# Kernel tuning notes

Hardware: AMD Instinct MI355X
Metric: run time of the kernel (lower is better)

Reference implementation:

```python
import jax, jax.numpy as jnp
import numpy as np

B, L, D, K = 16, 512, 512, 8
D2 = 2 * D
KS = 9
PAD = (KS - 1) // 2
EPS = 1e-5


def _conv_block(x, w, b, g, beta):
    # x: [B, L, D]; conv over time dim with 'same' padding, then LayerNorm over D, ReLU
    y = jax.lax.conv_general_dilated(
        x.transpose(0, 2, 1), w, window_strides=(1,), padding=[(PAD, PAD)],
        dimension_numbers=('NCH', 'OIH', 'NCH'))
    y = y.transpose(0, 2, 1) + b  # [B, L, D]
    mean = jnp.mean(y, axis=-1, keepdims=True)
    var = jnp.var(y, axis=-1, keepdims=True)
    y = (y - mean) * jax.lax.rsqrt(var + EPS) * g + beta
    return jax.nn.relu(y)


def _gru_scan(x, w_ih, w_hh, b_ih, b_hh):
    # x: [B, L, D]; torch GRUCell math, input = concat(x_t, h_{t-1}) per module
    def step(h, x_t):
        p = jnp.concatenate([x_t, h], axis=-1)          # [B, D + D2]
        gi = p @ w_ih.T + b_ih                          # [B, 3*D2]
        gh = h @ w_hh.T + b_hh
        ir, iz, inn = jnp.split(gi, 3, axis=-1)
        hr, hz, hn = jnp.split(gh, 3, axis=-1)
        r = jax.nn.sigmoid(ir + hr)
        z = jax.nn.sigmoid(iz + hz)
        n = jnp.tanh(inn + r * hn)
        h_new = (1.0 - z) * n + z * h
        return h_new, h_new

    h0 = jnp.zeros((x.shape[0], w_hh.shape[1]), x.dtype)
    _, hs = jax.lax.scan(step, h0, x.transpose(1, 0, 2))  # [L, B, D2]
    return hs.transpose(1, 0, 2)                           # [B, L, D2]


def setup_inputs() -> dict:
    key = jax.random.key(0)
    ks = jax.random.split(key, 12)
    n = lambda k, sh, s=0.02: jax.random.normal(k, sh, dtype=jnp.float32) * s
    return {
        'h_text': jax.random.normal(ks[0], (B, L, D), dtype=jnp.float32),
        'conv1_w': n(ks[1], (D, D, KS)), 'conv1_b': jnp.zeros((D,), jnp.float32),
        'ln1_g': jnp.ones((D,), jnp.float32), 'ln1_b': jnp.zeros((D,), jnp.float32),
        'conv2_w': n(ks[2], (D, D, KS)), 'conv2_b': jnp.zeros((D,), jnp.float32),
        'ln2_g': jnp.ones((D,), jnp.float32), 'ln2_b': jnp.zeros((D,), jnp.float32),
        'w_ih': n(ks[3], (3 * D2, D + D2)), 'w_hh': n(ks[4], (3 * D2, D2)),
        'b_ih': jnp.zeros((3 * D2,), jnp.float32), 'b_hh': jnp.zeros((3 * D2,), jnp.float32),
        'mdn_w_w': n(ks[5], (K, D2)), 'mdn_w_b': jnp.zeros((K,), jnp.float32),
        'mdn_sigma_w': n(ks[6], (K * D2, D2)), 'mdn_sigma_b': jnp.zeros((K * D2,), jnp.float32),
        'mdn_mu_w': n(ks[7], (K * D2, D2)), 'mdn_mu_b': jnp.zeros((K * D2,), jnp.float32),
    }


def reference(h_text, conv1_w, conv1_b, ln1_g, ln1_b, conv2_w, conv2_b, ln2_g, ln2_b,
              w_ih, w_hh, b_ih, b_hh, mdn_w_w, mdn_w_b, mdn_sigma_w, mdn_sigma_b,
              mdn_mu_w, mdn_mu_b):
    x = _conv_block(h_text, conv1_w, conv1_b, ln1_g, ln1_b)
    x = _conv_block(x, conv2_w, conv2_b, ln2_g, ln2_b)
    h = _gru_scan(x, w_ih, w_hh, b_ih, b_hh)                 # [B, L, 2D]
    w = jax.nn.softmax(h @ mdn_w_w.T + mdn_w_b, axis=-1)     # [B, L, K]
    sigma = jnp.exp(h @ mdn_sigma_w.T + mdn_sigma_b).reshape(B, L, K, D2)
    mu = (h @ mdn_mu_w.T + mdn_mu_b).reshape(B, L, K, D2)
    return (w, sigma, mu)
```

## Files before the change

### kernel.cpp

```cpp
#include <hip/hip_runtime.h>
#include <hip/hip_bf16.h>
#include <math.h>

#define BB 16
#define LL 512
#define DD 512
#define DD2 1024
#define KMIX 8
#define LPAD 520
#define GRU_KSTEPS 33

typedef __attribute__((ext_vector_type(8))) short short8;
typedef __attribute__((ext_vector_type(4))) float f32x4;
typedef unsigned short ushort;

__device__ __forceinline__ float bf2f(ushort u) {
  union { float f; unsigned i; } v; v.i = ((unsigned)u) << 16; return v.f;
}
__device__ __forceinline__ ushort f2bf(float f) {
  union { float f; unsigned i; } v; v.f = f;
  unsigned i = v.i;
  unsigned r = i + 0x7FFF + ((i >> 16) & 1);
  return (ushort)(r >> 16);
}

__global__ void k_zero_bf16(ushort* p, long n) {
  for (long i = blockIdx.x * 256 + threadIdx.x; i < n; i += (long)gridDim.x * 256) p[i] = 0;
}
__global__ void k_fill_xpad(const float* __restrict__ x, ushort* __restrict__ xp) {
  const long n = (long)BB * LPAD * DD;
  for (long i = blockIdx.x * 256 + threadIdx.x; i < n; i += (long)gridDim.x * 256) {
    int d = (int)(i & 511);
    long rest = i >> 9;
    int p = (int)(rest % LPAD);
    int b = (int)(rest / LPAD);
    float v = 0.f;
    if (p >= 4 && p < 516) v = x[((long)b * LL + (p - 4)) * DD + d];
    xp[i] = f2bf(v);
  }
}
__global__ void k_pack_convw(const float* __restrict__ w, ushort* __restrict__ wp) {
  const long n = (long)DD * DD * 9;
  for (long idx = blockIdx.x * 256 + threadIdx.x; idx < n; idx += (long)gridDim.x * 256) {
    int i = (int)(idx & 511);
    int o = (int)((idx >> 9) & 511);
    int k = (int)(idx >> 18);
    wp[idx] = f2bf(w[((long)o * DD + i) * 9 + k]);
  }
}
__global__ void k_pack_wihx(const float* __restrict__ w_ih, ushort* __restrict__ wp) {
  const long n = (long)3 * DD2 * DD;
  for (long idx = blockIdx.x * 256 + threadIdx.x; idx < n; idx += (long)gridDim.x * 256) {
    int i = (int)(idx & 511);
    int nr = (int)(idx >> 9);
    wp[idx] = f2bf(w_ih[(long)nr * 1536 + i]);
  }
}
__global__ void k_pack_bf16(const float* __restrict__ s, ushort* __restrict__ d, long n) {
  for (long i = blockIdx.x * 256 + threadIdx.x; i < n; i += (long)gridDim.x * 256) d[i] = f2bf(s[i]);
}
__global__ void k_pack_gru(const float* __restrict__ w_ih, const float* __restrict__ w_hh,
                           const float* __restrict__ b_hh, ushort* __restrict__ wp) {
  const long n = (long)64 * 6 * GRU_KSTEPS * 64 * 8;
  for (long idx = blockIdx.x * 256 + threadIdx.x; idx < n; idx += (long)gridDim.x * 256) {
    int j = (int)(idx & 7);
    int lane = (int)((idx >> 3) & 63);
    long r9 = idx >> 9;
    int ks = (int)(r9 % GRU_KSTEPS);
    long tmp = r9 / GRU_KSTEPS;
    int s = (int)(tmp % 6);
    int blk = (int)(tmp / 6);
    int k = ks * 32 + ((lane >> 4) << 3) + j;
    int u = blk * 16 + (lane & 15);
    float v = 0.f;
    if (s < 3) {
      if (k < 1024) v = w_ih[((long)(s * DD2 + u)) * 1536 + 512 + k];
    } else {
      int nr = (s - 3) * DD2 + u;
      if (k < 1024) v = w_hh[(long)nr * DD2 + k];
      else if (k == 1024) v = b_hh[nr];
    }
    wp[idx] = f2bf(v);
  }
}
__global__ void k_init_hbuf(ushort* hb, unsigned* flags) {
  int i = blockIdx.x * 256 + threadIdx.x;
  if (i < 16384) hb[i] = 0;
  if (i < 1024) flags[i] = 0u;
}

template <int MODE, int AMAP>
__global__ __launch_bounds__(256) void gemm128(
    const ushort* __restrict__ A, int lda, long segAoff,
    const ushort* __restrict__ Bt, int ldb, long segBoff,
    int nseg, int kseg, void* __restrict__ Cout, int ldc,
    const float* __restrict__ bias) {
  __shared__ ushort As[128 * 64];
  __shared__ ushort Bs[128 * 64];
  const int tid = threadIdx.x, lane = tid & 63, w = tid >> 6;
  const int wr = w >> 1, wc = w & 1;
  const int m0 = blockIdx.y * 128, n0 = blockIdx.x * 128;

  const ushort* Abase;
  if (AMAP == 1) {
    int b = m0 >> 9, l = m0 & 511;
    Abase = A + ((long)(b * LPAD + l)) * DD;
  } else {
    Abase = A + (long)m0 * lda;
  }
  const ushort* Bbase = Bt + (long)n0 * ldb;

  f32x4 acc[4][4];
#pragma unroll
  for (int i = 0; i < 4; i++)
#pragma unroll
    for (int j = 0; j < 4; j++) acc[i][j] = {0.f, 0.f, 0.f, 0.f};

  for (int seg = 0; seg < nseg; ++seg) {
    const ushort* Aseg = Abase + (long)seg * segAoff;
    const ushort* Bseg = Bbase + (long)seg * segBoff;
    for (int k0 = 0; k0 < kseg; k0 += 64) {
#pragma unroll
      for (int it = 0; it < 4; ++it) {
        int chunk = it * 256 + tid;
        int r = chunk >> 3, cc = chunk & 7;
        int sc = cc ^ (r & 7);
        *(short8*)&As[(size_t)chunk * 8] = *(const short8*)(Aseg + (long)r * lda + k0 + sc * 8);
        *(short8*)&Bs[(size_t)chunk * 8] = *(const short8*)(Bseg + (long)r * ldb + k0 + sc * 8);
      }
      __syncthreads();
#pragma unroll
      for (int kk = 0; kk < 2; ++kk) {
        short8 af[4], bfv[4];
#pragma unroll
        for (int m = 0; m < 4; m++) {
          int row = wr * 64 + m * 16 + (lane & 15);
          int ch = (kk * 4 + (lane >> 4)) ^ (row & 7);
          af[m] = *(const short8*)&As[(size_t)(row * 8 + ch) * 8];
        }
#pragma unroll
        for (int nn = 0; nn < 4; nn++) {
          int row = wc * 64 + nn * 16 + (lane & 15);
          int ch = (kk * 4 + (lane >> 4)) ^ (row & 7);
          bfv[nn] = *(const short8*)&Bs[(size_t)(row * 8 + ch) * 8];
        }
#pragma unroll
        for (int m = 0; m < 4; m++)
#pragma unroll
          for (int nn = 0; nn < 4; nn++)
            acc[m][nn] = __builtin_amdgcn_mfma_f32_16x16x32_bf16(af[m], bfv[nn], acc[m][nn], 0, 0, 0);
      }
      __syncthreads();
    }
  }
  float bvals[4];
#pragma unroll
  for (int nn = 0; nn < 4; nn++) {
    int c = n0 + wc * 64 + nn * 16 + (lane & 15);
    bvals[nn] = bias[c];
  }
#pragma unroll
  for (int m = 0; m < 4; m++) {
    int rbase = m0 + wr * 64 + m * 16 + ((lane >> 4) << 2);
#pragma unroll
    for (int nn = 0; nn < 4; nn++) {
      int c = n0 + wc * 64 + nn * 16 + (lane & 15);
#pragma unroll
      for (int j = 0; j < 4; j++) {
        float v = acc[m][nn][j] + bvals[nn];
        long off = (long)(rbase + j) * ldc + c;
        if (MODE == 0) ((float*)Cout)[off] = v;
        else if (MODE == 1) ((ushort*)Cout)[off] = f2bf(v);
        else if (MODE == 2) ((float*)Cout)[off] = v;
        else ((float*)Cout)[off] = expf(v);
      }
    }
  }
}

template <int DSTPAD>
__global__ __launch_bounds__(256) void ln_relu(
    const float* __restrict__ y, const float* __restrict__ g,
    const float* __restrict__ be, ushort* __restrict__ dst) {
  const int r = blockIdx.x, tid = threadIdx.x;
  float v0 = y[(long)r * DD + tid];
  float v1 = y[(long)r * DD + 256 + tid];
  float s = v0 + v1, sq = v0 * v0 + v1 * v1;
#pragma unroll
  for (int o = 32; o; o >>= 1) { s += __shfl_down(s, o); sq += __shfl_down(sq, o); }
  __shared__ float red[8];
  int w = tid >> 6, lane = tid & 63;
  if (lane == 0) { red[w] = s; red[4 + w] = sq; }
  __syncthreads();
  if (tid == 0) {
    float ts = 0.f, tq = 0.f;
#pragma unroll
    for (int i = 0; i < 4; i++) { ts += red[i]; tq += red[4 + i]; }
    red[0] = ts; red[1] = tq;
  }
  __syncthreads();
  float mean = red[0] * (1.f / 512.f);
  float var = red[1] * (1.f / 512.f) - mean * mean;
  float rs = rsqrtf(var + 1e-5f);
  long dbase;
  if (DSTPAD) { int b = r >> 9, l = r & 511; dbase = ((long)(b * LPAD + l + 4)) * DD; }
  else dbase = (long)r * DD;
  float o0 = fmaxf(0.f, (v0 - mean) * rs * g[tid] + be[tid]);
  float o1 = fmaxf(0.f, (v1 - mean) * rs * g[tid + 256] + be[tid + 256]);
  dst[dbase + tid] = f2bf(o0);
  dst[dbase + 256 + tid] = f2bf(o1);
}

__global__ __launch_bounds__(256, 1) void gru_scan(
    const ushort* __restrict__ Wp, const ushort* __restrict__ gix,
    const float* __restrict__ b_hh,
    ushort* __restrict__ hbuf, ushort* __restrict__ h_seq,
    unsigned* __restrict__ flags) {
  __shared__ float red[4 * 6 * 256];
  const int tid = threadIdx.x, lane = tid & 63, w = tid >> 6, blk = blockIdx.x;
  const int j_c = w;
  const int u_local = lane & 15;
  const int b = ((lane >> 4) << 2) + j_c;
  const int u = (blk << 4) + u_local;
  const int lanep = ((blk & 1) * 2 + (u_local >> 3)) * 16 + b;
  const long hout_off = ((long)(blk >> 1) * 64 + lanep) * 8 + (u_local & 7);
  const ushort* wpw = Wp + (long)blk * 6 * GRU_KSTEPS * 512 + (long)lane * 8;
  const float bhr = b_hh[u], bhz = b_hh[DD2 + u], bhn = b_hh[2 * DD2 + u];
  float hold = 0.f;

  short8 wreg0[8], wreg1[8], wreg2[8];
#pragma unroll
  for (int i = 0; i < 8; ++i) {
    const int ks = i * 4 + w;
    wreg0[i] = *(const short8*)(wpw + (long)(0 * GRU_KSTEPS + ks) * 512);
    wreg1[i] = *(const short8*)(wpw + (long)(1 * GRU_KSTEPS + ks) * 512);
    wreg2[i] = *(const short8*)(wpw + (long)(2 * GRU_KSTEPS + ks) * 512);
  }

  for (int t = 0; t < LL; ++t) {
    const long gr = ((long)b * LL + t) * 3072 + u;
    const float gx_r = bf2f(__builtin_nontemporal_load(gix + gr));
    const float gx_z = bf2f(__builtin_nontemporal_load(gix + gr + DD2));
    const float gx_n = bf2f(__builtin_nontemporal_load(gix + gr + 2 * DD2));

    if (t > 0) {
      if (w == 0) {
        const unsigned tgt = (unsigned)t;
        while (1) {
          unsigned f = __hip_atomic_load(&flags[lane << 4], __ATOMIC_RELAXED,
                                         __HIP_MEMORY_SCOPE_AGENT);
          if (__all((int)(f >= tgt))) break;
          __builtin_amdgcn_s_sleep(1);
        }
      }
      __syncthreads();
    }

    const ushort* hb = hbuf + ((long)t << 14);
    f32x4 acc0 = {0.f,0.f,0.f,0.f}, acc1 = acc0, acc2 = acc0,
          acc3 = acc0, acc4 = acc0, acc5 = acc0;
#pragma unroll
    for (int i = 0; i < 8; ++i) {
      const int ks = i * 4 + w;
      unsigned long long* ap = (unsigned long long*)(hb + (((long)ks * 64 + lane) << 3));
      union { unsigned long long q[2]; short8 v; } cv;
      cv.q[0] = __hip_atomic_load(ap,     __ATOMIC_RELAXED, __HIP_MEMORY_SCOPE_AGENT);
      cv.q[1] = __hip_atomic_load(ap + 1, __ATOMIC_RELAXED, __HIP_MEMORY_SCOPE_AGENT);
      short8 b3 = *(const short8*)(wpw + (long)(3 * GRU_KSTEPS + ks) * 512);
      short8 b4 = *(const short8*)(wpw + (long)(4 * GRU_KSTEPS + ks) * 512);
      short8 b5 = *(const short8*)(wpw + (long)(5 * GRU_KSTEPS + ks) * 512);
      acc0 = __builtin_amdgcn_mfma_f32_16x16x32_bf16(cv.v, wreg0[i], acc0, 0, 0, 0);
      acc1 = __builtin_amdgcn_mfma_f32_16x16x32_bf16(cv.v, wreg1[i], acc1, 0, 0, 0);
      acc2 = __builtin_amdgcn_mfma_f32_16x16x32_bf16(cv.v, wreg2[i], acc2, 0, 0, 0);
      acc3 = __builtin_amdgcn_mfma_f32_16x16x32_bf16(cv.v, b3, acc3, 0, 0, 0);
      acc4 = __builtin_amdgcn_mfma_f32_16x16x32_bf16(cv.v, b4, acc4, 0, 0, 0);
      acc5 = __builtin_amdgcn_mfma_f32_16x16x32_bf16(cv.v, b5, acc5, 0, 0, 0);
    }
#pragma unroll
    for (int j = 0; j < 4; ++j) {
      red[((w * 6 + 0) << 8) + (j << 6) + lane] = acc0[j];
      red[((w * 6 + 1) << 8) + (j << 6) + lane] = acc1[j];
      red[((w * 6 + 2) << 8) + (j << 6) + lane] = acc2[j];
      red[((w * 6 + 3) << 8) + (j << 6) + lane] = acc3[j];
      red[((w * 6 + 4) << 8) + (j << 6) + lane] = acc4[j];
      red[((w * 6 + 5) << 8) + (j << 6) + lane] = acc5[j];
    }
    __syncthreads();
    float v0 = 0.f, v1 = 0.f, v2 = 0.f, v3 = 0.f, v4 = 0.f, v5 = 0.f;
#pragma unroll
    for (int wv = 0; wv < 4; ++wv) {
      const int base = ((wv * 6) << 8) + (j_c << 6) + lane;
      v0 += red[base];
      v1 += red[base + 256];
      v2 += red[base + 512];
      v3 += red[base + 768];
      v4 += red[base + 1024];
      v5 += red[base + 1280];
    }
    const float rg = 1.f / (1.f + __expf(-(gx_r + v0 + v3 + bhr)));
    const float zg = 1.f / (1.f + __expf(-(gx_z + v1 + v4 + bhz)));
    const float nx = gx_n + v2 + rg * (v5 + bhn);
    const float ng = 1.f - 2.f / (__expf(2.f * nx) + 1.f);
    const float hn = (1.f - zg) * ng + zg * hold;
    hold = hn;
    const ushort h16 = f2bf(hn);
    h_seq[((long)b * LL + t) * DD2 + u] = h16;
    if (t < LL - 1) {
      __hip_atomic_store(hbuf + (((long)(t + 1)) << 14) + hout_off, h16,
                         __ATOMIC_RELAXED, __HIP_MEMORY_SCOPE_AGENT);
      __syncthreads();
      if (tid == 0)
        __hip_atomic_store(&flags[blk << 4], (unsigned)(t + 1), __ATOMIC_RELAXED,
                           __HIP_MEMORY_SCOPE_AGENT);
    }
  }
}

__global__ __launch_bounds__(256) void w_head(
    const ushort* __restrict__ h_seq, const float* __restrict__ ww,
    const float* __restrict__ wb, float* __restrict__ out) {
  const int tid = threadIdx.x, lane = tid & 63, w = tid >> 6;
  const long r = (long)blockIdx.x * 4 + w;
  float s[KMIX];
#pragma unroll
  for (int k = 0; k < KMIX; k++) s[k] = 0.f;
  for (int u = lane; u < DD2; u += 64) {
    float hv = bf2f(h_seq[r * DD2 + u]);
#pragma unroll
    for (int k = 0; k < KMIX; k++) s[k] += hv * ww[(long)k * DD2 + u];
  }
#pragma unroll
  for (int k = 0; k < KMIX; k++)
#pragma unroll
    for (int o = 32; o; o >>= 1) s[k] += __shfl_xor(s[k], o);
#pragma unroll
  for (int k = 0; k < KMIX; k++) s[k] += wb[k];
  float m = s[0];
#pragma unroll
  for (int k = 1; k < KMIX; k++) m = fmaxf(m, s[k]);
  float esum = 0.f;
#pragma unroll
  for (int k = 0; k < KMIX; k++) { s[k] = expf(s[k] - m); esum += s[k]; }
  float mine = 0.f;
#pragma unroll
  for (int k = 0; k < KMIX; k++) if (lane == k) mine = s[k];
  if (lane < KMIX) out[r * KMIX + lane] = mine / esum;
}

extern "C" void kernel_launch(void* const* d_in, const int* in_sizes, int n_in,
                              void* d_out, int out_size, void* d_ws, size_t ws_size,
                              hipStream_t stream) {
  const float* h_text     = (const float*)d_in[0];
  const float* conv1_w    = (const float*)d_in[1];
  const float* conv1_b    = (const float*)d_in[2];
  const float* ln1_g      = (const float*)d_in[3];
  const float* ln1_b      = (const float*)d_in[4];
  const float* conv2_w    = (const float*)d_in[5];
  const float* conv2_b    = (const float*)d_in[6];
  const float* ln2_g      = (const float*)d_in[7];
  const float* ln2_b      = (const float*)d_in[8];
  const float* w_ih       = (const float*)d_in[9];
  const float* w_hh       = (const float*)d_in[10];
  const float* b_ih       = (const float*)d_in[11];
  const float* b_hh       = (const float*)d_in[12];
  const float* mdn_w_w    = (const float*)d_in[13];
  const float* mdn_w_b    = (const float*)d_in[14];
  const float* mdn_sig_w  = (const float*)d_in[15];
  const float* mdn_sig_b  = (const float*)d_in[16];
  const float* mdn_mu_w   = (const float*)d_in[17];
  const float* mdn_mu_b   = (const float*)d_in[18];
  float* out = (float*)d_out;

  char* ws = (char*)d_ws;
  size_t off = 0;
  auto take = [&](size_t bytes) {
    void* p = ws + off;
    off += (bytes + 255) & ~(size_t)255;
    return p;
  };
  ushort* xpad1  = (ushort*)take((size_t)BB * LPAD * DD * 2);
  ushort* xpad2  = (ushort*)take((size_t)BB * LPAD * DD * 2);
  ushort* wpack1 = (ushort*)take((size_t)DD * DD * 9 * 2);
  ushort* wpack2 = (ushort*)take((size_t)DD * DD * 9 * 2);
  float*  ybuf   = (float*) take((size_t)BB * LL * DD * 4);
  ushort* x2     = (ushort*)take((size_t)BB * LL * DD * 2);
  ushort* wihx   = (ushort*)take((size_t)3 * DD2 * DD * 2);
  ushort* gix    = (ushort*)take((size_t)BB * LL * 3 * DD2 * 2);
  ushort* Wp     = (ushort*)take((size_t)64 * 6 * GRU_KSTEPS * 64 * 8 * 2);
  ushort* hseq   = (ushort*)take((size_t)BB * LL * DD2 * 2);
  ushort* mdnmu  = (ushort*)take((size_t)KMIX * DD2 * DD2 * 2);
  ushort* mdnsg  = (ushort*)take((size_t)KMIX * DD2 * DD2 * 2);
  ushort* hbuf   = (ushort*)take((size_t)512 * 16384 * 2);
  unsigned* flags = (unsigned*)take(64 * 16 * 4);

  const long sigma_off = (long)BB * LL * KMIX;
  const long mu_off    = sigma_off + (long)BB * LL * KMIX * DD2;

  k_fill_xpad<<<2048, 256, 0, stream>>>(h_text, xpad1);
  k_zero_bf16<<<2048, 256, 0, stream>>>(xpad2, (long)BB * LPAD * DD);
  k_pack_convw<<<2048, 256, 0, stream>>>(conv1_w, wpack1);
  k_pack_convw<<<2048, 256, 0, stream>>>(conv2_w, wpack2);
  k_pack_wihx<<<2048, 256, 0, stream>>>(w_ih, wihx);
  k_pack_gru<<<2048, 256, 0, stream>>>(w_ih, w_hh, b_hh, Wp);
  k_pack_bf16<<<2048, 256, 0, stream>>>(mdn_mu_w, mdnmu, (long)KMIX * DD2 * DD2);
  k_pack_bf16<<<2048, 256, 0, stream>>>(mdn_sig_w, mdnsg, (long)KMIX * DD2 * DD2);
  k_init_hbuf<<<64, 256, 0, stream>>>(hbuf, flags);

  gemm128<0, 1><<<dim3(4, 64), 256, 0, stream>>>(xpad1, DD, DD, wpack1, DD, (long)DD * DD, 9, DD,
                                                 ybuf, DD, conv1_b);
  ln_relu<1><<<BB * LL, 256, 0, stream>>>(ybuf, ln1_g, ln1_b, xpad2);

  gemm128<0, 1><<<dim3(4, 64), 256, 0, stream>>>(xpad2, DD, DD, wpack2, DD, (long)DD * DD, 9, DD,
                                                 ybuf, DD, conv2_b);
  ln_relu<0><<<BB * LL, 256, 0, stream>>>(ybuf, ln2_g, ln2_b, x2);

  gemm128<1, 0><<<dim3(24, 64), 256, 0, stream>>>(x2, DD, 0, wihx, DD, 0, 1, DD,
                                                  gix, 3 * DD2, b_ih);

  gru_scan<<<64, 256, 0, stream>>>(Wp, gix, b_hh, hbuf, hseq, flags);

  gemm128<3, 0><<<dim3(64, 64), 256, 0, stream>>>(hseq, DD2, 0, mdnsg, DD2, 0, 1, DD2,
                                                  out + sigma_off, KMIX * DD2, mdn_sig_b);
  gemm128<2, 0><<<dim3(64, 64), 256, 0, stream>>>(hseq, DD2, 0, mdnmu, DD2, 0, 1, DD2,
                                                  out + mu_off, KMIX * DD2, mdn_mu_b);
  w_head<<<BB * LL / 4, 256, 0, stream>>>(hseq, mdn_w_w, mdn_w_b, out);
}
```

Before: 2.078 ms.

## Use per-wave release flags in GRU scan to drop block-wide barriers

Each wave now publishes its own progress flag with release semantics. Every wave polls all 256 per-wave flags directly, using two 64-bit loads per lane, instead of wave 0 polling per-block flags and then broadcasting through __syncthreads. This removes two block barriers per timestep on the serial recurrence path. The h_seq store becomes nontemporal and moves after the flag publish so it is off the critical path. The risk is more polling traffic and relying on the remaining shared-memory barriers to order reuse of the reduction buffer across steps.

Result: slower. 5.008 ms (+141.0%).

```diff
diff --git a/kernel.cpp b/kernel.cpp
--- a/kernel.cpp
+++ b/kernel.cpp
@@ -215,7 +215,7 @@
     const ushort* __restrict__ Wp, const ushort* __restrict__ gix,
     const float* __restrict__ b_hh,
     ushort* __restrict__ hbuf, ushort* __restrict__ h_seq,
-    unsigned* __restrict__ flags) {
+    unsigned* __restrict__ wflags) {
   __shared__ float red[4 * 6 * 256];
   const int tid = threadIdx.x, lane = tid & 63, w = tid >> 6, blk = blockIdx.x;
   const int j_c = w;
@@ -244,16 +244,20 @@
     const float gx_n = bf2f(__builtin_nontemporal_load(gix + gr + 2 * DD2));
 
     if (t > 0) {
-      if (w == 0) {
-        const unsigned tgt = (unsigned)t;
-        while (1) {
-          unsigned f = __hip_atomic_load(&flags[lane << 4], __ATOMIC_RELAXED,
-                                         __HIP_MEMORY_SCOPE_AGENT);
-          if (__all((int)(f >= tgt))) break;
-          __builtin_amdgcn_s_sleep(1);
-        }
+      const unsigned tgt = (unsigned)t;
+      while (1) {
+        unsigned long long q0 = __hip_atomic_load(
+            (const unsigned long long*)&wflags[lane << 4],
+            __ATOMIC_RELAXED, __HIP_MEMORY_SCOPE_AGENT);
+        unsigned long long q1 = __hip_atomic_load(
+            (const unsigned long long*)&wflags[(lane << 4) + 2],
+            __ATOMIC_RELAXED, __HIP_MEMORY_SCOPE_AGENT);
+        const unsigned m0 = (unsigned)q0, m1 = (unsigned)(q0 >> 32);
+        const unsigned m2 = (unsigned)q1, m3 = (unsigned)(q1 >> 32);
+        const bool ok = (m0 >= tgt) & (m1 >= tgt) & (m2 >= tgt) & (m3 >= tgt);
+        if (__all((int)ok)) break;
+        __builtin_amdgcn_s_sleep(1);
       }
-      __syncthreads();
     }
 
     const ushort* hb = hbuf + ((long)t << 14);
@@ -304,15 +308,14 @@
     const float hn = (1.f - zg) * ng + zg * hold;
     hold = hn;
     const ushort h16 = f2bf(hn);
-    h_seq[((long)b * LL + t) * DD2 + u] = h16;
     if (t < LL - 1) {
       __hip_atomic_store(hbuf + (((long)(t + 1)) << 14) + hout_off, h16,
                          __ATOMIC_RELAXED, __HIP_MEMORY_SCOPE_AGENT);
-      __syncthreads();
-      if (tid == 0)
-        __hip_atomic_store(&flags[blk << 4], (unsigned)(t + 1), __ATOMIC_RELAXED,
-                           __HIP_MEMORY_SCOPE_AGENT);
-    }
+      if (lane == 0)
+        __hip_atomic_store(&wflags[(blk << 4) + w], (unsigned)(t + 1),
+                           __ATOMIC_RELEASE, __HIP_MEMORY_SCOPE_AGENT);
+    }
+    __builtin_nontemporal_store(h16, h_seq + ((long)b * LL + t) * DD2 + u);
   }
 }
 
@@ -391,7 +394,7 @@
   ushort* mdnmu  = (ushort*)take((size_t)KMIX * DD2 * DD2 * 2);
   ushort* mdnsg  = (ushort*)take((size_t)KMIX * DD2 * DD2 * 2);
   ushort* hbuf   = (ushort*)take((size_t)512 * 16384 * 2);
-  unsigned* flags = (unsigned*)take(64 * 16 * 4);
+  unsigned* wflags = (unsigned*)take(64 * 16 * 4);
 
   const long sigma_off = (long)BB * LL * KMIX;
   const long mu_off    = sigma_off + (long)BB * LL * KMIX * DD2;
@@ -404,7 +407,7 @@
   k_pack_gru<<<2048, 256, 0, stream>>>(w_ih, w_hh, b_hh, Wp);
   k_pack_bf16<<<2048, 256, 0, stream>>>(mdn_mu_w, mdnmu, (long)KMIX * DD2 * DD2);
   k_pack_bf16<<<2048, 256, 0, stream>>>(mdn_sig_w, mdnsg, (long)KMIX * DD2 * DD2);
-  k_init_hbuf<<<64, 256, 0, stream>>>(hbuf, flags);
+  k_init_hbuf<<<64, 256, 0, stream>>>(hbuf, wflags);
 
   gemm128<0, 1><<<dim3(4, 64), 256, 0, stream>>>(xpad1, DD, DD, wpack1, DD, (long)DD * DD, 9, DD,
                                                  ybuf, DD, conv1_b);
@@ -417,7 +420,7 @@
   gemm128<1, 0><<<dim3(24, 64), 256, 0, stream>>>(x2, DD, 0, wihx, DD, 0, 1, DD,
                                                   gix, 3 * DD2, b_ih);
 
-  gru_scan<<<64, 256, 0, stream>>>(Wp, gix, b_hh, hbuf, hseq, flags);
+  gru_scan<<<64, 256, 0, stream>>>(Wp, gix, b_hh, hbuf, hseq, wflags);
 
   gemm128<3, 0><<<dim3(64, 64), 256, 0, stream>>>(hseq, DD2, 0, mdnsg, DD2, 0, 1, DD2,
                                                   out + sigma_off, KMIX * DD2, mdn_sig_b);
```

## Replace per-block flag barrier in GRU scan with tagged hidden-state words

Applied to the files above, without the earlier changes.

Each hidden-state value is now stored as a 32-bit word carrying the bf16 value plus a timestep tag. Consumers spin on the data itself until every tag matches, instead of waiting on per-block flags after a __syncthreads. This removes the producer-side barrier and the separate flag round-trip from the serial critical path. All six gate weight slices are also kept in registers rather than reloading three of them every step. The cost is twice the hbuf traffic, 64 extra live registers for the polled words plus the added weight registers, and busy polling without sleep.

New measurement: 5.199 ms. +150.1%, slower.

```diff
diff --git a/kernel.cpp b/kernel.cpp
--- a/kernel.cpp
+++ b/kernel.cpp
@@ -83,10 +83,9 @@
     wp[idx] = f2bf(v);
   }
 }
-__global__ void k_init_hbuf(ushort* hb, unsigned* flags) {
+__global__ void k_init_hbuf(unsigned* hb) {
   int i = blockIdx.x * 256 + threadIdx.x;
-  if (i < 16384) hb[i] = 0;
-  if (i < 1024) flags[i] = 0u;
+  if (i < 16384) hb[i] = 0u;
 }
 
 template <int MODE, int AMAP>
@@ -214,8 +213,7 @@
 __global__ __launch_bounds__(256, 1) void gru_scan(
     const ushort* __restrict__ Wp, const ushort* __restrict__ gix,
     const float* __restrict__ b_hh,
-    ushort* __restrict__ hbuf, ushort* __restrict__ h_seq,
-    unsigned* __restrict__ flags) {
+    unsigned* __restrict__ hbuf, ushort* __restrict__ h_seq) {
   __shared__ float red[4 * 6 * 256];
   const int tid = threadIdx.x, lane = tid & 63, w = tid >> 6, blk = blockIdx.x;
   const int j_c = w;
@@ -228,13 +226,16 @@
   const float bhr = b_hh[u], bhz = b_hh[DD2 + u], bhn = b_hh[2 * DD2 + u];
   float hold = 0.f;
 
-  short8 wreg0[8], wreg1[8], wreg2[8];
+  short8 wr0[8], wr1[8], wr2[8], wr3[8], wr4[8], wr5[8];
 #pragma unroll
   for (int i = 0; i < 8; ++i) {
     const int ks = i * 4 + w;
-    wreg0[i] = *(const short8*)(wpw + (long)(0 * GRU_KSTEPS + ks) * 512);
-    wreg1[i] = *(const short8*)(wpw + (long)(1 * GRU_KSTEPS + ks) * 512);
-    wreg2[i] = *(const short8*)(wpw + (long)(2 * GRU_KSTEPS + ks) * 512);
+    wr0[i] = *(const short8*)(wpw + (long)(0 * GRU_KSTEPS + ks) * 512);
+    wr1[i] = *(const short8*)(wpw + (long)(1 * GRU_KSTEPS + ks) * 512);
+    wr2[i] = *(const short8*)(wpw + (long)(2 * GRU_KSTEPS + ks) * 512);
+    wr3[i] = *(const short8*)(wpw + (long)(3 * GRU_KSTEPS + ks) * 512);
+    wr4[i] = *(const short8*)(wpw + (long)(4 * GRU_KSTEPS + ks) * 512);
+    wr5[i] = *(const short8*)(wpw + (long)(5 * GRU_KSTEPS + ks) * 512);
   }
 
   for (int t = 0; t < LL; ++t) {
@@ -243,38 +244,39 @@
     const float gx_z = bf2f(__builtin_nontemporal_load(gix + gr + DD2));
     const float gx_n = bf2f(__builtin_nontemporal_load(gix + gr + 2 * DD2));
 
-    if (t > 0) {
-      if (w == 0) {
-        const unsigned tgt = (unsigned)t;
-        while (1) {
-          unsigned f = __hip_atomic_load(&flags[lane << 4], __ATOMIC_RELAXED,
-                                         __HIP_MEMORY_SCOPE_AGENT);
-          if (__all((int)(f >= tgt))) break;
-          __builtin_amdgcn_s_sleep(1);
-        }
+    unsigned* hb = hbuf + ((long)t << 14);
+    const unsigned tagv = (unsigned)t & 0xFFFFu;
+    unsigned dv[64];
+    while (true) {
+      unsigned bad = 0u;
+#pragma unroll
+      for (int i = 0; i < 8; ++i) {
+        const int ks = i * 4 + w;
+        unsigned* ap = hb + (((long)ks * 64 + lane) << 3);
+#pragma unroll
+        for (int j = 0; j < 8; ++j)
+          dv[i * 8 + j] = __hip_atomic_load(ap + j, __ATOMIC_RELAXED,
+                                            __HIP_MEMORY_SCOPE_AGENT);
       }
-      __syncthreads();
-    }
-
-    const ushort* hb = hbuf + ((long)t << 14);
+#pragma unroll
+      for (int q = 0; q < 64; ++q) bad |= (dv[q] ^ tagv) & 0xFFFFu;
+      if (__all((int)(bad == 0u))) break;
+    }
+
     f32x4 acc0 = {0.f,0.f,0.f,0.f}, acc1 = acc0, acc2 = acc0,
           acc3 = acc0, acc4 = acc0, acc5 = acc0;
 #pragma unroll
     for (int i = 0; i < 8; ++i) {
-      const int ks = i * 4 + w;
-      unsigned long long* ap = (unsigned long long*)(hb + (((long)ks * 64 + lane) << 3));
-      union { unsigned long long q[2]; short8 v; } cv;
-      cv.q[0] = __hip_atomic_load(ap,     __ATOMIC_RELAXED, __HIP_MEMORY_SCOPE_AGENT);
-      cv.q[1] = __hip_atomic_load(ap + 1, __ATOMIC_RELAXED, __HIP_MEMORY_SCOPE_AGENT);
-      short8 b3 = *(const short8*)(wpw + (long)(3 * GRU_KSTEPS + ks) * 512);
-      short8 b4 = *(const short8*)(wpw + (long)(4 * GRU_KSTEPS + ks) * 512);
-      short8 b5 = *(const short8*)(wpw + (long)(5 * GRU_KSTEPS + ks) * 512);
-      acc0 = __builtin_amdgcn_mfma_f32_16x16x32_bf16(cv.v, wreg0[i], acc0, 0, 0, 0);
-      acc1 = __builtin_amdgcn_mfma_f32_16x16x32_bf16(cv.v, wreg1[i], acc1, 0, 0, 0);
-      acc2 = __builtin_amdgcn_mfma_f32_16x16x32_bf16(cv.v, wreg2[i], acc2, 0, 0, 0);
-      acc3 = __builtin_amdgcn_mfma_f32_16x16x32_bf16(cv.v, b3, acc3, 0, 0, 0);
-      acc4 = __builtin_amdgcn_mfma_f32_16x16x32_bf16(cv.v, b4, acc4, 0, 0, 0);
-      acc5 = __builtin_amdgcn_mfma_f32_16x16x32_bf16(cv.v, b5, acc5, 0, 0, 0);
+      union { unsigned u[4]; short8 v; } cv;
+#pragma unroll
+      for (int p = 0; p < 4; ++p)
+        cv.u[p] = (dv[i * 8 + 2 * p] >> 16) | (dv[i * 8 + 2 * p + 1] & 0xFFFF0000u);
+      acc0 = __builtin_amdgcn_mfma_f32_16x16x32_bf16(cv.v, wr0[i], acc0, 0, 0, 0);
+      acc1 = __builtin_amdgcn_mfma_f32_16x16x32_bf16(cv.v, wr1[i], acc1, 0, 0, 0);
+      acc2 = __builtin_amdgcn_mfma_f32_16x16x32_bf16(cv.v, wr2[i], acc2, 0, 0, 0);
+      acc3 = __builtin_amdgcn_mfma_f32_16x16x32_bf16(cv.v, wr3[i], acc3, 0, 0, 0);
+      acc4 = __builtin_amdgcn_mfma_f32_16x16x32_bf16(cv.v, wr4[i], acc4, 0, 0, 0);
+      acc5 = __builtin_amdgcn_mfma_f32_16x16x32_bf16(cv.v, wr5[i], acc5, 0, 0, 0);
     }
 #pragma unroll
     for (int j = 0; j < 4; ++j) {
@@ -304,15 +306,12 @@
     const float hn = (1.f - zg) * ng + zg * hold;
     hold = hn;
     const ushort h16 = f2bf(hn);
-    h_seq[((long)b * LL + t) * DD2 + u] = h16;
     if (t < LL - 1) {
-      __hip_atomic_store(hbuf + (((long)(t + 1)) << 14) + hout_off, h16,
+      const unsigned pv = ((unsigned)h16 << 16) | ((unsigned)(t + 1) & 0xFFFFu);
+      __hip_atomic_store(hbuf + (((long)(t + 1)) << 14) + hout_off, pv,
                          __ATOMIC_RELAXED, __HIP_MEMORY_SCOPE_AGENT);
-      __syncthreads();
-      if (tid == 0)
-        __hip_atomic_store(&flags[blk << 4], (unsigned)(t + 1), __ATOMIC_RELAXED,
-                           __HIP_MEMORY_SCOPE_AGENT);
-    }
+    }
+    __builtin_nontemporal_store(h16, h_seq + ((long)b * LL + t) * DD2 + u);
   }
 }
 
@@ -390,8 +389,7 @@
   ushort* hseq   = (ushort*)take((size_t)BB * LL * DD2 * 2);
   ushort* mdnmu  = (ushort*)take((size_t)KMIX * DD2 * DD2 * 2);
   ushort* mdnsg  = (ushort*)take((size_t)KMIX * DD2 * DD2 * 2);
-  ushort* hbuf   = (ushort*)take((size_t)512 * 16384 * 2);
-  unsigned* flags = (unsigned*)take(64 * 16 * 4);
+  unsigned* hbuf = (unsigned*)take((size_t)512 * 16384 * 4);
 
   const long sigma_off = (long)BB * LL * KMIX;
   const long mu_off    = sigma_off + (long)BB * LL * KMIX * DD2;
@@ -404,7 +402,7 @@
   k_pack_gru<<<2048, 256, 0, stream>>>(w_ih, w_hh, b_hh, Wp);
   k_pack_bf16<<<2048, 256, 0, stream>>>(mdn_mu_w, mdnmu, (long)KMIX * DD2 * DD2);
   k_pack_bf16<<<2048, 256, 0, stream>>>(mdn_sig_w, mdnsg, (long)KMIX * DD2 * DD2);
-  k_init_hbuf<<<64, 256, 0, stream>>>(hbuf, flags);
+  k_init_hbuf<<<64, 256, 0, stream>>>(hbuf);
 
   gemm128<0, 1><<<dim3(4, 64), 256, 0, stream>>>(xpad1, DD, DD, wpack1, DD, (long)DD * DD, 9, DD,
                                                  ybuf, DD, conv1_b);
@@ -417,7 +415,7 @@
   gemm128<1, 0><<<dim3(24, 64), 256, 0, stream>>>(x2, DD, 0, wihx, DD, 0, 1, DD,
                                                   gix, 3 * DD2, b_ih);
 
-  gru_scan<<<64, 256, 0, stream>>>(Wp, gix, b_hh, hbuf, hseq, flags);
+  gru_scan<<<64, 256, 0, stream>>>(Wp, gix, b_hh, hbuf, hseq);
 
   gemm128<3, 0><<<dim3(64, 64), 256, 0, stream>>>(hseq, DD2, 0, mdnsg, DD2, 0, 1, DD2,
                                                   out + sigma_off, KMIX * DD2, mdn_sig_b);
```

## Keep all GRU weights in registers and relayout gate inputs for scan

Applied to the files above, without the earlier changes.

The recurrent GRU scan kernel now loads all six gate weight slices into registers once, instead of reloading three of them from global memory every timestep. The input-gate GEMM gains a new output mode that writes gix in a per-timestep, per-block tiled layout, so each scan step reads its gate inputs from a contiguous chunk. Sync flags are packed densely instead of padded 16 apart, the spin sleep is raised, and h_seq is written with nontemporal stores. Holding all weights in registers raises register pressure in the single-block-per-CU scan and may cause spills. Dense flags may also add cache-line contention between blocks.

New measurement: 3.120 ms. 50.1% more time.

```diff
diff --git a/kernel.cpp b/kernel.cpp
--- a/kernel.cpp
+++ b/kernel.cpp
@@ -86,7 +86,7 @@
 __global__ void k_init_hbuf(ushort* hb, unsigned* flags) {
   int i = blockIdx.x * 256 + threadIdx.x;
   if (i < 16384) hb[i] = 0;
-  if (i < 1024) flags[i] = 0u;
+  if (i < 256) flags[i] = 0u;
 }
 
 template <int MODE, int AMAP>
@@ -172,7 +172,13 @@
         if (MODE == 0) ((float*)Cout)[off] = v;
         else if (MODE == 1) ((ushort*)Cout)[off] = f2bf(v);
         else if (MODE == 2) ((float*)Cout)[off] = v;
-        else ((float*)Cout)[off] = expf(v);
+        else if (MODE == 3) ((float*)Cout)[off] = expf(v);
+        else {
+          int r = rbase + j;
+          int bb = r >> 9, tt = r & 511, ss = c >> 10, uu = c & 1023;
+          long o2 = ((((long)(tt * 64 + (uu >> 4))) * 3 + ss) << 8) + (bb << 4) + (uu & 15);
+          ((ushort*)Cout)[o2] = f2bf(v);
+        }
       }
     }
   }
@@ -212,7 +218,7 @@
 }
 
 __global__ __launch_bounds__(256, 1) void gru_scan(
-    const ushort* __restrict__ Wp, const ushort* __restrict__ gix,
+    const ushort* __restrict__ Wp, const ushort* __restrict__ gix2,
     const float* __restrict__ b_hh,
     ushort* __restrict__ hbuf, ushort* __restrict__ h_seq,
     unsigned* __restrict__ flags) {
@@ -228,29 +234,33 @@
   const float bhr = b_hh[u], bhz = b_hh[DD2 + u], bhn = b_hh[2 * DD2 + u];
   float hold = 0.f;
 
-  short8 wreg0[8], wreg1[8], wreg2[8];
+  short8 wr0[8], wr1[8], wr2[8], wr3[8], wr4[8], wr5[8];
 #pragma unroll
   for (int i = 0; i < 8; ++i) {
     const int ks = i * 4 + w;
-    wreg0[i] = *(const short8*)(wpw + (long)(0 * GRU_KSTEPS + ks) * 512);
-    wreg1[i] = *(const short8*)(wpw + (long)(1 * GRU_KSTEPS + ks) * 512);
-    wreg2[i] = *(const short8*)(wpw + (long)(2 * GRU_KSTEPS + ks) * 512);
-  }
-
+    wr0[i] = *(const short8*)(wpw + (long)(0 * GRU_KSTEPS + ks) * 512);
+    wr1[i] = *(const short8*)(wpw + (long)(1 * GRU_KSTEPS + ks) * 512);
+    wr2[i] = *(const short8*)(wpw + (long)(2 * GRU_KSTEPS + ks) * 512);
+    wr3[i] = *(const short8*)(wpw + (long)(3 * GRU_KSTEPS + ks) * 512);
+    wr4[i] = *(const short8*)(wpw + (long)(4 * GRU_KSTEPS + ks) * 512);
+    wr5[i] = *(const short8*)(wpw + (long)(5 * GRU_KSTEPS + ks) * 512);
+  }
+
+  const int gofs = (b << 4) + u_local;
   for (int t = 0; t < LL; ++t) {
-    const long gr = ((long)b * LL + t) * 3072 + u;
-    const float gx_r = bf2f(__builtin_nontemporal_load(gix + gr));
-    const float gx_z = bf2f(__builtin_nontemporal_load(gix + gr + DD2));
-    const float gx_n = bf2f(__builtin_nontemporal_load(gix + gr + 2 * DD2));
+    const long gbase = ((long)(t * 64 + blk) * 3) << 8;
+    const float gx_r = bf2f(__builtin_nontemporal_load(gix2 + gbase + gofs));
+    const float gx_z = bf2f(__builtin_nontemporal_load(gix2 + gbase + 256 + gofs));
+    const float gx_n = bf2f(__builtin_nontemporal_load(gix2 + gbase + 512 + gofs));
 
     if (t > 0) {
       if (w == 0) {
         const unsigned tgt = (unsigned)t;
         while (1) {
-          unsigned f = __hip_atomic_load(&flags[lane << 4], __ATOMIC_RELAXED,
+          unsigned f = __hip_atomic_load(&flags[lane], __ATOMIC_RELAXED,
                                          __HIP_MEMORY_SCOPE_AGENT);
           if (__all((int)(f >= tgt))) break;
-          __builtin_amdgcn_s_sleep(1);
+          __builtin_amdgcn_s_sleep(2);
         }
       }
       __syncthreads();
@@ -266,15 +276,12 @@
       union { unsigned long long q[2]; short8 v; } cv;
       cv.q[0] = __hip_atomic_load(ap,     __ATOMIC_RELAXED, __HIP_MEMORY_SCOPE_AGENT);
       cv.q[1] = __hip_atomic_load(ap + 1, __ATOMIC_RELAXED, __HIP_MEMORY_SCOPE_AGENT);
-      short8 b3 = *(const short8*)(wpw + (long)(3 * GRU_KSTEPS + ks) * 512);
-      short8 b4 = *(const short8*)(wpw + (long)(4 * GRU_KSTEPS + ks) * 512);
-      short8 b5 = *(const short8*)(wpw + (long)(5 * GRU_KSTEPS + ks) * 512);
-      acc0 = __builtin_amdgcn_mfma_f32_16x16x32_bf16(cv.v, wreg0[i], acc0, 0, 0, 0);
-      acc1 = __builtin_amdgcn_mfma_f32_16x16x32_bf16(cv.v, wreg1[i], acc1, 0, 0, 0);
-      acc2 = __builtin_amdgcn_mfma_f32_16x16x32_bf16(cv.v, wreg2[i], acc2, 0, 0, 0);
-      acc3 = __builtin_amdgcn_mfma_f32_16x16x32_bf16(cv.v, b3, acc3, 0, 0, 0);
-      acc4 = __builtin_amdgcn_mfma_f32_16x16x32_bf16(cv.v, b4, acc4, 0, 0, 0);
-      acc5 = __builtin_amdgcn_mfma_f32_16x16x32_bf16(cv.v, b5, acc5, 0, 0, 0);
+      acc0 = __builtin_amdgcn_mfma_f32_16x16x32_bf16(cv.v, wr0[i], acc0, 0, 0, 0);
+      acc1 = __builtin_amdgcn_mfma_f32_16x16x32_bf16(cv.v, wr1[i], acc1, 0, 0, 0);
+      acc2 = __builtin_amdgcn_mfma_f32_16x16x32_bf16(cv.v, wr2[i], acc2, 0, 0, 0);
+      acc3 = __builtin_amdgcn_mfma_f32_16x16x32_bf16(cv.v, wr3[i], acc3, 0, 0, 0);
+      acc4 = __builtin_amdgcn_mfma_f32_16x16x32_bf16(cv.v, wr4[i], acc4, 0, 0, 0);
+      acc5 = __builtin_amdgcn_mfma_f32_16x16x32_bf16(cv.v, wr5[i], acc5, 0, 0, 0);
     }
 #pragma unroll
     for (int j = 0; j < 4; ++j) {
@@ -304,13 +311,13 @@
     const float hn = (1.f - zg) * ng + zg * hold;
     hold = hn;
     const ushort h16 = f2bf(hn);
-    h_seq[((long)b * LL + t) * DD2 + u] = h16;
+    __builtin_nontemporal_store(h16, h_seq + ((long)b * LL + t) * DD2 + u);
     if (t < LL - 1) {
       __hip_atomic_store(hbuf + (((long)(t + 1)) << 14) + hout_off, h16,
                          __ATOMIC_RELAXED, __HIP_MEMORY_SCOPE_AGENT);
       __syncthreads();
       if (tid == 0)
-        __hip_atomic_store(&flags[blk << 4], (unsigned)(t + 1), __ATOMIC_RELAXED,
+        __hip_atomic_store(&flags[blk], (unsigned)(t + 1), __ATOMIC_RELAXED,
                            __HIP_MEMORY_SCOPE_AGENT);
     }
   }
@@ -391,7 +398,7 @@
   ushort* mdnmu  = (ushort*)take((size_t)KMIX * DD2 * DD2 * 2);
   ushort* mdnsg  = (ushort*)take((size_t)KMIX * DD2 * DD2 * 2);
   ushort* hbuf   = (ushort*)take((size_t)512 * 16384 * 2);
-  unsigned* flags = (unsigned*)take(64 * 16 * 4);
+  unsigned* flags = (unsigned*)take(256 * 4);
 
   const long sigma_off = (long)BB * LL * KMIX;
   const long mu_off    = sigma_off + (long)BB * LL * KMIX * DD2;
@@ -414,7 +421,7 @@
                                                  ybuf, DD, conv2_b);
   ln_relu<0><<<BB * LL, 256, 0, stream>>>(ybuf, ln2_g, ln2_b, x2);
 
-  gemm128<1, 0><<<dim3(24, 64), 256, 0, stream>>>(x2, DD, 0, wihx, DD, 0, 1, DD,
+  gemm128<4, 0><<<dim3(24, 64), 256, 0, stream>>>(x2, DD, 0, wihx, DD, 0, 1, DD,
                                                   gix, 3 * DD2, b_ih);
 
   gru_scan<<<64, 256, 0, stream>>>(Wp, gix, b_hh, hbuf, hseq, flags);
```
